# Optimization experiments

Measured on AMD Instinct MI355X. Metric: run time of the kernel, lower is better.

Reference implementation:

```python
import jax, jax.numpy as jnp
import numpy as np

DIM = 4096
BATCH = 8192
NUM_LAYERS = 6
STRENGTHS = (0.1, 0.1, 0.05)  # entail, contra, neutral
EPS_NORM = 1e-12  # torch F.normalize eps
MAX_NORM = 10.0


def _normalize(x, axis=-1):
    n = jnp.linalg.norm(x, axis=axis, keepdims=True)
    return x / jnp.maximum(n, EPS_NORM)


def setup_inputs() -> dict:
    key = jax.random.key(0)
    k0, k1, k2, k3 = jax.random.split(key, 4)
    return {
        "h0": jax.random.normal(k0, (BATCH, DIM), dtype=jnp.float32),
        "anchor_entail": jax.random.normal(k1, (DIM,), dtype=jnp.float32),
        "anchor_contra": jax.random.normal(k2, (DIM,), dtype=jnp.float32),
        "anchor_neutral": jax.random.normal(k3, (DIM,), dtype=jnp.float32),
    }


def reference(h0, anchor_entail, anchor_contra, anchor_neutral):
    # Normalized fixed anchor directions, stacked [3, dim] (E, C, N)
    dirs = jnp.stack([
        _normalize(anchor_entail, axis=0),
        _normalize(anchor_contra, axis=0),
        _normalize(anchor_neutral, axis=0),
    ])  # [3, dim]
    strengths = jnp.asarray(STRENGTHS, dtype=h0.dtype)  # [3]

    def step(h, _):
        h_n = _normalize(h)                         # [B, dim]
        align = jnp.einsum("bd,kd->bk", h_n, dirs)  # [B, 3]
        div = 1.0 - align                           # divergence_from_alignment
        tens = jnp.maximum(div, 0.0)                # tension (clamp min=0)
        # normalized direction away from each anchor: [B, 3, dim]
        vec = _normalize(h[:, None, :] - dirs[None, :, :])
        force = jnp.einsum("bk,bkd->bd", strengths[None, :] * div, vec)
        h = h - force
        h_norm = jnp.linalg.norm(h, axis=-1, keepdims=True)
        h = jnp.where(h_norm > MAX_NORM, h * (MAX_NORM / (h_norm + 1e-8)), h)
        return h, (align, div, tens)

    h_final, (aligns, divs, tensions) = jax.lax.scan(step, h0, None, length=NUM_LAYERS)
    # traces: [num_layers, B, 3] with anchor order (entail, contra, neutral)
    return h_final, aligns, divs, tensions
```

## Files before the change

kernel.cpp:

```cpp
#include <hip/hip_runtime.h>


constexpr int DIM = 4096;
constexpr int BATCH = 8192;
constexpr int NLAYERS = 6;
constexpr int TPB = 256;
constexpr int VPT = DIM / (TPB * 4);

constexpr size_t HOUT = (size_t)BATCH * DIM;
constexpr size_t TRACE = (size_t)NLAYERS * BATCH * 3;
constexpr size_t OFF_ALIGN = HOUT;
constexpr size_t OFF_DIV   = HOUT + TRACE;
constexpr size_t OFF_TENS  = HOUT + 2 * TRACE;

__device__ float g_gram[12];

__device__ __forceinline__ float frcp(float x) { return __builtin_amdgcn_rcpf(x); }
__device__ __forceinline__ float frsq(float x) { return __builtin_amdgcn_rsqf(x); }
__device__ __forceinline__ float fsq(float x)  { return __builtin_amdgcn_sqrtf(x); }

__device__ __forceinline__ float wave_red(float v) {
#pragma unroll
  for (int off = 32; off > 0; off >>= 1) v += __shfl_down(v, off, 64);
  return v;
}

__global__ __launch_bounds__(TPB) void gram_kernel(
    const float* __restrict__ an0, const float* __restrict__ an1,
    const float* __restrict__ an2) {
  const int tid = threadIdx.x;
  float r[6];
#pragma unroll
  for (int i = 0; i < 6; ++i) r[i] = 0.f;
#pragma unroll
  for (int j = 0; j < VPT; ++j) {
    const int idx = (tid + j * TPB) * 4;
    const float4 x = *(const float4*)(an0 + idx);
    const float4 y = *(const float4*)(an1 + idx);
    const float4 z = *(const float4*)(an2 + idx);
    r[0] += x.x*x.x + x.y*x.y + x.z*x.z + x.w*x.w;
    r[1] += y.x*y.x + y.y*y.y + y.z*y.z + y.w*y.w;
    r[2] += z.x*z.x + z.y*z.y + z.z*z.z + z.w*z.w;
    r[3] += x.x*y.x + x.y*y.y + x.z*y.z + x.w*y.w;
    r[4] += x.x*z.x + x.y*z.y + x.z*z.z + x.w*z.w;
    r[5] += y.x*z.x + y.y*z.y + y.z*z.z + y.w*z.w;
  }
  __shared__ float lds[4][6];
  const int lane = tid & 63, wv = tid >> 6;
#pragma unroll
  for (int i = 0; i < 6; ++i) r[i] = wave_red(r[i]);
  if (lane == 0) {
#pragma unroll
    for (int i = 0; i < 6; ++i) lds[wv][i] = r[i];
  }
  __syncthreads();
  if (tid == 0) {
#pragma unroll
    for (int i = 0; i < 6; ++i)
      r[i] = lds[0][i] + lds[1][i] + lds[2][i] + lds[3][i];
    const float n0 = fmaxf(sqrtf(r[0]), 1e-12f);
    const float n1 = fmaxf(sqrtf(r[1]), 1e-12f);
    const float n2 = fmaxf(sqrtf(r[2]), 1e-12f);
    g_gram[0] = 1.f / n0;
    g_gram[1] = 1.f / n1;
    g_gram[2] = 1.f / n2;
    g_gram[3] = r[0] / (n0 * n0);
    g_gram[4] = r[1] / (n1 * n1);
    g_gram[5] = r[2] / (n2 * n2);
    g_gram[6] = r[3] / (n0 * n1);
    g_gram[7] = r[4] / (n0 * n2);
    g_gram[8] = r[5] / (n1 * n2);
  }
}

__global__ __launch_bounds__(TPB) void fused_kernel(
    const float* __restrict__ h0,
    const float* __restrict__ an0, const float* __restrict__ an1,
    const float* __restrict__ an2, float* __restrict__ out) {
  const int b = blockIdx.x;
  const int tid = threadIdx.x;
  const int lane = tid & 63, wv = tid >> 6;
  const float* hrow = h0 + (size_t)b * DIM;

  float4 hv[VPT];
  float r0 = 0.f, r1 = 0.f, r2 = 0.f, r3 = 0.f;
#pragma unroll
  for (int j = 0; j < VPT; ++j) {
    const int idx = (tid + j * TPB) * 4;
    hv[j] = *(const float4*)(hrow + idx);
    const float4 x = *(const float4*)(an0 + idx);
    const float4 y = *(const float4*)(an1 + idx);
    const float4 z = *(const float4*)(an2 + idx);
    const float4 h = hv[j];
    r0 += h.x*h.x + h.y*h.y + h.z*h.z + h.w*h.w;
    r1 += h.x*x.x + h.y*x.y + h.z*x.z + h.w*x.w;
    r2 += h.x*y.x + h.y*y.y + h.z*y.z + h.w*y.w;
    r3 += h.x*z.x + h.y*z.y + h.z*z.z + h.w*z.w;
  }

  __shared__ float lds[4][4];
  r0 = wave_red(r0); r1 = wave_red(r1); r2 = wave_red(r2); r3 = wave_red(r3);
  if (lane == 0) {
    lds[wv][0] = r0; lds[wv][1] = r1; lds[wv][2] = r2; lds[wv][3] = r3;
  }
  __syncthreads();

  float s  = lds[0][0] + lds[1][0] + lds[2][0] + lds[3][0];
  float d0 = lds[0][1] + lds[1][1] + lds[2][1] + lds[3][1];
  float d1 = lds[0][2] + lds[1][2] + lds[2][2] + lds[3][2];
  float d2 = lds[0][3] + lds[1][3] + lds[2][3] + lds[3][3];

  const float rn0 = g_gram[0], rn1 = g_gram[1], rn2 = g_gram[2];
  const float G00 = g_gram[3], G11 = g_gram[4], G22 = g_gram[5];
  const float G01 = g_gram[6], G02 = g_gram[7], G12 = g_gram[8];
  d0 *= rn0; d1 *= rn1; d2 *= rn2;

  float A = 1.f, B0 = 0.f, B1 = 0.f, B2 = 0.f;
  float* tr_al = out + OFF_ALIGN + (size_t)b * 3;
  float* tr_dv = out + OFF_DIV   + (size_t)b * 3;
  float* tr_tn = out + OFF_TENS  + (size_t)b * 3;

#pragma unroll
  for (int l = 0; l < NLAYERS; ++l) {
    const float rhn = frsq(fmaxf(s, 1e-24f));
    const float al0 = d0 * rhn, al1 = d1 * rhn, al2 = d2 * rhn;
    const float dv0 = 1.f - al0, dv1 = 1.f - al1, dv2 = 1.f - al2;
    const float rr0 = frsq(fmaxf(s - 2.f*d0 + G00, 1e-24f));
    const float rr1 = frsq(fmaxf(s - 2.f*d1 + G11, 1e-24f));
    const float rr2 = frsq(fmaxf(s - 2.f*d2 + G22, 1e-24f));
    const float c0 = 0.10f * dv0 * rr0;
    const float c1 = 0.10f * dv1 * rr1;
    const float c2 = 0.05f * dv2 * rr2;
    if (tid == 0) {
      const size_t o = (size_t)l * (BATCH * 3);
      tr_al[o+0] = al0; tr_al[o+1] = al1; tr_al[o+2] = al2;
      tr_dv[o+0] = dv0; tr_dv[o+1] = dv1; tr_dv[o+2] = dv2;
      tr_tn[o+0] = fmaxf(dv0, 0.f); tr_tn[o+1] = fmaxf(dv1, 0.f);
      tr_tn[o+2] = fmaxf(dv2, 0.f);
    }
    const float a = 1.f - (c0 + c1 + c2);
    const float dn0 = a*d0 + c0*G00 + c1*G01 + c2*G02;
    const float dn1 = a*d1 + c0*G01 + c1*G11 + c2*G12;
    const float dn2 = a*d2 + c0*G02 + c1*G12 + c2*G22;
    float sn = a*a*s + 2.f*a*(c0*d0 + c1*d1 + c2*d2)
             + c0*c0*G00 + c1*c1*G11 + c2*c2*G22
             + 2.f*(c0*c1*G01 + c0*c2*G02 + c1*c2*G12);
    A = a * A;
    B0 = a*B0 + c0; B1 = a*B1 + c1; B2 = a*B2 + c2;
    s = sn; d0 = dn0; d1 = dn1; d2 = dn2;
    const float hn2 = fsq(s);
    if (hn2 > 10.0f) {
      const float sc = 10.0f * frcp(hn2 + 1e-8f);
      A *= sc; B0 *= sc; B1 *= sc; B2 *= sc;
      d0 *= sc; d1 *= sc; d2 *= sc;
      s *= sc * sc;
    }
  }
  const float w0 = B0 * rn0, w1 = B1 * rn1, w2 = B2 * rn2;

  float* orow = out + (size_t)b * DIM;
#pragma unroll
  for (int j = 0; j < VPT; ++j) {
    const int idx = (tid + j * TPB) * 4;
    const float4 x = *(const float4*)(an0 + idx);
    const float4 y = *(const float4*)(an1 + idx);
    const float4 z = *(const float4*)(an2 + idx);
    const float4 h = hv[j];
    float4 o;
    o.x = A * h.x + w0 * x.x + w1 * y.x + w2 * z.x;
    o.y = A * h.y + w0 * x.y + w1 * y.y + w2 * z.y;
    o.z = A * h.z + w0 * x.z + w1 * y.z + w2 * z.z;
    o.w = A * h.w + w0 * x.w + w1 * y.w + w2 * z.w;
    *(float4*)(orow + idx) = o;
  }
}

extern "C" void kernel_launch(void* const* d_in, const int* in_sizes, int n_in,
                              void* d_out, int out_size, void* d_ws, size_t ws_size,
                              hipStream_t stream) {
  const float* h0  = (const float*)d_in[0];
  const float* an0 = (const float*)d_in[1];
  const float* an1 = (const float*)d_in[2];
  const float* an2 = (const float*)d_in[3];
  float* out = (float*)d_out;
  (void)d_ws; (void)ws_size;
  gram_kernel<<<1, TPB, 0, stream>>>(an0, an1, an2);
  fused_kernel<<<BATCH, TPB, 0, stream>>>(h0, an0, an1, an2, out);
}
```

Baseline: 259.7 us.

## Assign one row per wavefront to remove block-level reduction and barrier

Each wavefront now processes a whole batch row, so a block covers four rows and the grid shrinks by four. The cross-wave LDS reduction and __syncthreads are replaced by xor-shuffle all-reduces inside the wave. Each lane now holds 16 float4 of h in registers instead of 4, which raises register pressure and may lower occupancy for this memory-bound kernel.

```diff
diff --git a/kernel.cpp b/kernel.cpp
--- a/kernel.cpp
+++ b/kernel.cpp
@@ -5,7 +5,9 @@
 constexpr int BATCH = 8192;
 constexpr int NLAYERS = 6;
 constexpr int TPB = 256;
-constexpr int VPT = DIM / (TPB * 4);
+constexpr int WPB = TPB / 64;
+constexpr int GRID = BATCH / WPB;
+constexpr int FPW = DIM / (64 * 4);
 
 constexpr size_t HOUT = (size_t)BATCH * DIM;
 constexpr size_t TRACE = (size_t)NLAYERS * BATCH * 3;
@@ -25,6 +27,12 @@
   return v;
 }
 
+__device__ __forceinline__ float wave_allred(float v) {
+#pragma unroll
+  for (int off = 32; off > 0; off >>= 1) v += __shfl_xor(v, off, 64);
+  return v;
+}
+
 __global__ __launch_bounds__(TPB) void gram_kernel(
     const float* __restrict__ an0, const float* __restrict__ an1,
     const float* __restrict__ an2) {
@@ -33,7 +41,7 @@
 #pragma unroll
   for (int i = 0; i < 6; ++i) r[i] = 0.f;
 #pragma unroll
-  for (int j = 0; j < VPT; ++j) {
+  for (int j = 0; j < DIM / (TPB * 4); ++j) {
     const int idx = (tid + j * TPB) * 4;
     const float4 x = *(const float4*)(an0 + idx);
     const float4 y = *(const float4*)(an1 + idx);
@@ -77,16 +85,16 @@
     const float* __restrict__ h0,
     const float* __restrict__ an0, const float* __restrict__ an1,
     const float* __restrict__ an2, float* __restrict__ out) {
-  const int b = blockIdx.x;
-  const int tid = threadIdx.x;
-  const int lane = tid & 63, wv = tid >> 6;
+  const int lane = threadIdx.x & 63;
+  const int wv = threadIdx.x >> 6;
+  const int b = blockIdx.x * WPB + wv;
   const float* hrow = h0 + (size_t)b * DIM;
 
-  float4 hv[VPT];
+  float4 hv[FPW];
   float r0 = 0.f, r1 = 0.f, r2 = 0.f, r3 = 0.f;
 #pragma unroll
-  for (int j = 0; j < VPT; ++j) {
-    const int idx = (tid + j * TPB) * 4;
+  for (int j = 0; j < FPW; ++j) {
+    const int idx = (j * 64 + lane) * 4;
     hv[j] = *(const float4*)(hrow + idx);
     const float4 x = *(const float4*)(an0 + idx);
     const float4 y = *(const float4*)(an1 + idx);
@@ -98,17 +106,10 @@
     r3 += h.x*z.x + h.y*z.y + h.z*z.z + h.w*z.w;
   }
 
-  __shared__ float lds[4][4];
-  r0 = wave_red(r0); r1 = wave_red(r1); r2 = wave_red(r2); r3 = wave_red(r3);
-  if (lane == 0) {
-    lds[wv][0] = r0; lds[wv][1] = r1; lds[wv][2] = r2; lds[wv][3] = r3;
-  }
-  __syncthreads();
-
-  float s  = lds[0][0] + lds[1][0] + lds[2][0] + lds[3][0];
-  float d0 = lds[0][1] + lds[1][1] + lds[2][1] + lds[3][1];
-  float d1 = lds[0][2] + lds[1][2] + lds[2][2] + lds[3][2];
-  float d2 = lds[0][3] + lds[1][3] + lds[2][3] + lds[3][3];
+  float s  = wave_allred(r0);
+  float d0 = wave_allred(r1);
+  float d1 = wave_allred(r2);
+  float d2 = wave_allred(r3);
 
   const float rn0 = g_gram[0], rn1 = g_gram[1], rn2 = g_gram[2];
   const float G00 = g_gram[3], G11 = g_gram[4], G22 = g_gram[5];
@@ -131,7 +132,7 @@
     const float c0 = 0.10f * dv0 * rr0;
     const float c1 = 0.10f * dv1 * rr1;
     const float c2 = 0.05f * dv2 * rr2;
-    if (tid == 0) {
+    if (lane == 0) {
       const size_t o = (size_t)l * (BATCH * 3);
       tr_al[o+0] = al0; tr_al[o+1] = al1; tr_al[o+2] = al2;
       tr_dv[o+0] = dv0; tr_dv[o+1] = dv1; tr_dv[o+2] = dv2;
@@ -160,8 +161,8 @@
 
   float* orow = out + (size_t)b * DIM;
 #pragma unroll
-  for (int j = 0; j < VPT; ++j) {
-    const int idx = (tid + j * TPB) * 4;
+  for (int j = 0; j < FPW; ++j) {
+    const int idx = (j * 64 + lane) * 4;
     const float4 x = *(const float4*)(an0 + idx);
     const float4 y = *(const float4*)(an1 + idx);
     const float4 z = *(const float4*)(an2 + idx);
@@ -185,5 +186,5 @@
   float* out = (float*)d_out;
   (void)d_ws; (void)ws_size;
   gram_kernel<<<1, TPB, 0, stream>>>(an0, an1, an2);
-  fused_kernel<<<BATCH, TPB, 0, stream>>>(h0, an0, an1, an2, out);
+  fused_kernel<<<GRID, TPB, 0, stream>>>(h0, an0, an1, an2, out);
 }
```

New measurement: 253.5 us. 1.02x faster.
